# Kernel tuning notes

Measured on AMD Instinct MI355X. Metric: run time of the kernel, lower is better.

## Reference

```python
import jax, jax.numpy as jnp
import numpy as np


def setup_inputs() -> dict:
    key = jax.random.key(0)
    ks = jax.random.split(key, 5)
    t, b, s, d = 4, 4, 1024, 512
    x = jax.random.normal(ks[0], (t, b, s, d), dtype=jnp.float32)
    wq = jax.random.normal(ks[1], (d, d), dtype=jnp.float32) * 0.02
    wk = jax.random.normal(ks[2], (d, d), dtype=jnp.float32) * 0.02
    wv = jax.random.normal(ks[3], (d, d), dtype=jnp.float32) * 0.02
    wo = jax.random.normal(ks[4], (d, d), dtype=jnp.float32) * 0.02
    z = jnp.zeros((d,), dtype=jnp.float32)
    return {"x": x, "wq": wq, "bq": z, "wk": wk, "bk": z, "wv": wv,
            "bv": z, "wo": wo, "bo": z, "num_heads": 8}


def reference(x, wq, bq, wk, bk, wv, bv, wo, bo, num_heads):
    t, b, s, d = x.shape
    dh = d // num_heads
    # QKV projections (torch Linear stores weight as [out,in]; here weights are
    # random square matrices so x @ w + b is the same math)
    q = x @ wq + bq
    k = x @ wk + bk
    v = x @ wv + bv
    # Faithful to source: plain row-major view to (t*b*h, s, dh) WITHOUT
    # transposing a head axis (this mixes seq blocks into the batch-of-heads dim)
    q = q.reshape(t * b * num_heads, s, dh)
    k = k.reshape(t * b * num_heads, s, dh)
    v = v.reshape(t * b * num_heads, s, dh)
    scale = 1.0 / jnp.sqrt(jnp.float32(dh))
    scores = jnp.einsum('bqd,bkd->bqk', q, k) * scale  # [t*b*h, s, s]
    attn = jax.nn.softmax(scores, axis=-1)
    out = jnp.einsum('bqk,bkd->bqd', attn, v)  # [t*b*h, s, dh]
    out = out.reshape(t, b, s, d)
    return out @ wo + bo
```

## Files before the change

kernel.cpp:

```cpp
#include <hip/hip_runtime.h>

typedef __bf16 bf16;
typedef __bf16 bf16x4 __attribute__((ext_vector_type(4)));
typedef __bf16 bf16x8 __attribute__((ext_vector_type(8)));
typedef float  f32x4  __attribute__((ext_vector_type(4)));

#define MFMA16(a, b, c) __builtin_amdgcn_mfma_f32_16x16x32_bf16((a), (b), (c), 0, 0, 0)
#define SW(row, g) (((row) << 6) + ((((g) ^ ((row) & 7))) << 3))

#define QSCALE 0.1803368801111137f

typedef __attribute__((address_space(3))) uint32_t       lds_u32_t;
typedef const __attribute__((address_space(1))) uint32_t glob_u32_t;

__device__ __forceinline__ void ld_lds16(const bf16* g, bf16* l) {
    __builtin_amdgcn_global_load_lds((glob_u32_t*)g, (lds_u32_t*)l, 16, 0, 0);
}

__global__ __launch_bounds__(256) void prep(
    const float* __restrict__ X,
    const float* __restrict__ wq, const float* __restrict__ wk,
    const float* __restrict__ wv, const float* __restrict__ wo,
    bf16* __restrict__ Xb, bf16* __restrict__ wqkvT, bf16* __restrict__ woT)
{
    int bid = blockIdx.x;
    if (bid < 4096) {
        size_t i = ((size_t)bid * 256 + threadIdx.x) * 8;
        const f32x4* s = (const f32x4*)(X + i);
        f32x4 a = s[0], b = s[1];
        bf16x8 o;
        for (int e = 0; e < 4; e++) { o[e] = (bf16)a[e]; o[e + 4] = (bf16)b[e]; }
        *(bf16x8*)(Xb + i) = o;
    } else {
        int idx = (bid - 4096) * 256 + threadIdx.x;
        int which = idx >> 15;
        int r = idx & 32767;
        int kg = r >> 9, n = r & 511;
        const float* w = (which == 0) ? wq : (which == 1) ? wk : (which == 2) ? wv : wo;
        bf16x8 o;
        for (int e = 0; e < 8; e++) o[e] = (bf16)w[(size_t)(kg * 8 + e) * 512 + n];
        bf16* dst = ((which < 3) ? (wqkvT + (size_t)which * 262144) : woT) + (size_t)n * 512 + kg * 8;
        *(bf16x8*)dst = o;
    }
}

__global__ __launch_bounds__(256, 4) void gemm_qkv(
    const bf16* __restrict__ Xb, const bf16* __restrict__ WT,
    const float* __restrict__ bq, const float* __restrict__ bk,
    const float* __restrict__ bv,
    bf16* __restrict__ Q, bf16* __restrict__ K, bf16* __restrict__ V)
{
    __shared__ char smem[34816];
    bf16* As = (bf16*)smem;
    bf16* Bs = (bf16*)(smem + 16384);

    const int t = threadIdx.x;
    const int lane = t & 63, wid = t >> 6;
    const int wr = wid >> 1, wc = wid & 1;
    const int lr = lane & 15, quad = lane >> 4;
    const int bid = blockIdx.x;
    const int xcd = bid & 7, j0 = bid >> 3;
    const int m0 = (xcd * 16 + (j0 & 15)) * 128;
    const int x = j0 >> 4;
    const int which = x >> 2;
    const int n0 = (x & 3) * 128;
    const bf16* Wt = WT + (size_t)which * 262144;

    f32x4 zf = {0.f, 0.f, 0.f, 0.f};
    f32x4 acc[4][4];
    for (int i = 0; i < 4; i++)
        for (int jj = 0; jj < 4; jj++) acc[i][jj] = zf;

    const int srow = t >> 3;
    const int sg = (t & 7) ^ (srow & 7);
    const bf16* gA = Xb + (size_t)(m0 + srow) * 512 + sg * 8;
    const bf16* gB = Wt + (size_t)(n0 + srow) * 512 + sg * 8;
    bf16* lA = As + t * 8;
    bf16* lB = Bs + t * 8;

    for (int k0 = 0; k0 < 512; k0 += 64) {
        for (int p = 0; p < 4; p++) {
            ld_lds16(gA + k0 + p * 32 * 512, lA + p * 2048);
            ld_lds16(gB + k0 + p * 32 * 512, lB + p * 2048);
        }
        __syncthreads();
        for (int kk = 0; kk < 2; ++kk) {
            bf16x8 af[4], bf_[4];
            for (int i = 0; i < 4; i++)
                af[i] = *(const bf16x8*)&As[SW(wr * 64 + i * 16 + lr, kk * 4 + quad)];
            for (int jj = 0; jj < 4; jj++)
                bf_[jj] = *(const bf16x8*)&Bs[SW(wc * 64 + jj * 16 + lr, kk * 4 + quad)];
            for (int i = 0; i < 4; i++)
                for (int jj = 0; jj < 4; jj++)
                    acc[i][jj] = MFMA16(af[i], bf_[jj], acc[i][jj]);
        }
        __syncthreads();
    }

    bf16* OUT = (which == 0) ? Q : (which == 1) ? K : V;
    const float* bias = (which == 0) ? bq : (which == 1) ? bk : bv;
    const float qs = (which == 0) ? QSCALE : 1.0f;

    bf16* Ep = (bf16*)smem + wid * 4352;
    for (int jj = 0; jj < 4; jj++) {
        int n = n0 + wc * 64 + jj * 16 + lr;
        float bb = bias[n];
        for (int i = 0; i < 4; i++) {
            int row = i * 16 + quad * 4;
            for (int r = 0; r < 4; r++)
                Ep[(row + r) * 68 + jj * 16 + lr] = (bf16)((acc[i][jj][r] + bb) * qs);
        }
    }
    bf16* wO = OUT + (size_t)(m0 + wr * 64) * 512 + n0 + wc * 64;
    for (int s = 0; s < 8; s++) {
        int row = s * 8 + (lane >> 3), g = lane & 7;
        *(bf16x8*)(wO + (size_t)row * 512 + g * 8) = *(const bf16x8*)&Ep[row * 68 + g * 8];
    }
}

__global__ __launch_bounds__(256, 4) void gemm_out(
    const bf16* __restrict__ A, const bf16* __restrict__ WoT,
    const float* __restrict__ bo, float* __restrict__ OUT)
{
    __shared__ char smem[34816];
    bf16* As = (bf16*)smem;
    bf16* Bs = (bf16*)(smem + 16384);

    const int t = threadIdx.x;
    const int lane = t & 63, wid = t >> 6;
    const int wr = wid >> 1, wc = wid & 1;
    const int lr = lane & 15, quad = lane >> 4;
    const int bid = blockIdx.x;
    const int xcd = bid & 7, j0 = bid >> 3;
    const int m0 = (xcd * 16 + (j0 & 15)) * 128;
    const int n0 = (j0 >> 4) * 128;

    f32x4 zf = {0.f, 0.f, 0.f, 0.f};
    f32x4 acc[4][4];
    for (int i = 0; i < 4; i++)
        for (int jj = 0; jj < 4; jj++) acc[i][jj] = zf;

    const int srow = t >> 3;
    const int sg = (t & 7) ^ (srow & 7);
    const bf16* gA = A + (size_t)(m0 + srow) * 512 + sg * 8;
    const bf16* gB = WoT + (size_t)(n0 + srow) * 512 + sg * 8;
    bf16* lA = As + t * 8;
    bf16* lB = Bs + t * 8;

    for (int k0 = 0; k0 < 512; k0 += 64) {
        for (int p = 0; p < 4; p++) {
            ld_lds16(gA + k0 + p * 32 * 512, lA + p * 2048);
            ld_lds16(gB + k0 + p * 32 * 512, lB + p * 2048);
        }
        __syncthreads();
        for (int kk = 0; kk < 2; ++kk) {
            bf16x8 af[4], bf_[4];
            for (int i = 0; i < 4; i++)
                af[i] = *(const bf16x8*)&As[SW(wr * 64 + i * 16 + lr, kk * 4 + quad)];
            for (int jj = 0; jj < 4; jj++)
                bf_[jj] = *(const bf16x8*)&Bs[SW(wc * 64 + jj * 16 + lr, kk * 4 + quad)];
            for (int i = 0; i < 4; i++)
                for (int jj = 0; jj < 4; jj++)
                    acc[i][jj] = MFMA16(af[i], bf_[jj], acc[i][jj]);
        }
        __syncthreads();
    }

    float bb[4];
    for (int jj = 0; jj < 4; jj++) bb[jj] = bo[n0 + wc * 64 + jj * 16 + lr];

    float* Ef = (float*)smem + wid * 2112;
    for (int h = 0; h < 2; h++) {
        for (int jj = 0; jj < 4; jj++)
            for (int ii = 0; ii < 2; ii++) {
                int i = h * 2 + ii;
                int row = ii * 16 + quad * 4;
                for (int r = 0; r < 4; r++)
                    Ef[(row + r) * 66 + jj * 16 + lr] = acc[i][jj][r] + bb[jj];
            }
        float* wO = OUT + (size_t)(m0 + wr * 64 + h * 32) * 512 + n0 + wc * 64;
        for (int s = 0; s < 8; s++) {
            int row = s * 4 + (lane >> 4), c = (lane & 15) * 4;
            *(f32x4*)(wO + (size_t)row * 512 + c) = *(const f32x4*)&Ef[row * 66 + c];
        }
        __syncthreads();
    }
}

__global__ __launch_bounds__(256) void transpose_v(
    const bf16* __restrict__ V, bf16* __restrict__ VT)
{
    __shared__ bf16 L[64 * 72];
    const int t = threadIdx.x;
    const int b = blockIdx.y, kb = blockIdx.x;
    const bf16* src = V + ((size_t)b * 1024 + (size_t)kb * 64) * 64;
    const int row = t >> 2, c0 = (t & 3) * 16;
    *(bf16x8*)&L[row * 72 + c0]     = *(const bf16x8*)(src + row * 64 + c0);
    *(bf16x8*)&L[row * 72 + c0 + 8] = *(const bf16x8*)(src + row * 64 + c0 + 8);
    __syncthreads();
    bf16x8 o0, o1;
    for (int e = 0; e < 8; e++) {
        o0[e] = L[(c0 + e) * 72 + row];
        o1[e] = L[(c0 + 8 + e) * 72 + row];
    }
    bf16* dst = VT + ((size_t)b * 64 + row) * 1024 + (size_t)kb * 64 + c0;
    *(bf16x8*)dst       = o0;
    *(bf16x8*)(dst + 8) = o1;
}

__global__ __launch_bounds__(256, 4) void attn(
    const bf16* __restrict__ Q, const bf16* __restrict__ K,
    const bf16* __restrict__ VT, bf16* __restrict__ O)
{
    __shared__ char smem[32768];
    bf16* Kt = (bf16*)smem;
    bf16* Vt = (bf16*)(smem + 8192);
    bf16* Pt = (bf16*)(smem + 16384);

    const int t = threadIdx.x, lane = t & 63, wid = t >> 6;
    const int lr = lane & 15, quad = lane >> 4;
    const int bid = blockIdx.x;
    const int batch = (bid & 7) * 16 + ((bid >> 3) & 15);
    const int q0 = (bid >> 7) * 128;
    const bf16* Qb = Q + (size_t)batch * 65536;
    const bf16* Kb = K + (size_t)batch * 65536;
    const bf16* Vb = VT + (size_t)batch * 65536;

    bf16x8 qf[2][2];
    for (int jt = 0; jt < 2; jt++)
        for (int kk = 0; kk < 2; kk++)
            qf[jt][kk] = *(const bf16x8*)(Qb + (size_t)(q0 + wid * 32 + jt * 16 + lr) * 64 + kk * 32 + quad * 8);

    float lsum[2] = {0.f, 0.f};
    f32x4 zf = {0.f, 0.f, 0.f, 0.f};
    f32x4 oacc[2][4];
    for (int a = 0; a < 2; a++)
        for (int b = 0; b < 4; b++) oacc[a][b] = zf;

    const int vrow = t >> 2, vg = (t & 3) * 2;
    const bf16* gK = Kb + (size_t)vrow * 64 + (t & 3) * 16;
    const bf16* gV = Vb + (size_t)vrow * 1024 + (t & 3) * 16;

    bf16x8 kr0 = ((const bf16x8*)gK)[0], kr1 = ((const bf16x8*)gK)[1];
    bf16x8 vr0 = ((const bf16x8*)gV)[0], vr1 = ((const bf16x8*)gV)[1];

    for (int kt = 0; kt < 16; ++kt) {
        __syncthreads();
        *(bf16x8*)&Kt[SW(vrow, vg)]     = kr0;
        *(bf16x8*)&Kt[SW(vrow, vg + 1)] = kr1;
        *(bf16x8*)&Vt[SW(vrow, vg)]     = vr0;
        *(bf16x8*)&Vt[SW(vrow, vg + 1)] = vr1;
        __syncthreads();

        if (kt < 15) {
            const bf16x8* nK = (const bf16x8*)(gK + (kt + 1) * 4096);
            const bf16x8* nV = (const bf16x8*)(gV + (kt + 1) * 64);
            kr0 = nK[0]; kr1 = nK[1];
            vr0 = nV[0]; vr1 = nV[1];
        }

        f32x4 sacc[4][2];
        for (int i = 0; i < 4; i++)
            for (int jt = 0; jt < 2; jt++) sacc[i][jt] = zf;
        for (int kk = 0; kk < 2; ++kk) {
            bf16x8 af[4];
            for (int i = 0; i < 4; i++)
                af[i] = *(const bf16x8*)&Kt[SW(i * 16 + lr, kk * 4 + quad)];
            for (int i = 0; i < 4; i++)
                for (int jt = 0; jt < 2; jt++)
                    sacc[i][jt] = MFMA16(af[i], qf[jt][kk], sacc[i][jt]);
        }

        for (int jt = 0; jt < 2; jt++) {
            const int qrow = wid * 32 + jt * 16 + lr;
            const int pbase = (qrow << 6) + (quad & 1) * 4;
            float ss = 0.f;
            for (int i = 0; i < 4; i++) {
                bf16x4 pb;
                for (int r = 0; r < 4; r++) {
                    float p = __builtin_amdgcn_exp2f(sacc[i][jt][r]);
                    ss += p;
                    pb[r] = (bf16)p;
                }
                *(bf16x4*)&Pt[pbase + ((((i * 2 + (quad >> 1)) ^ (qrow & 7))) << 3)] = pb;
            }
            lsum[jt] += ss;
        }

        for (int kk = 0; kk < 2; ++kk) {
            bf16x8 ap[2], bv_[4];
            for (int mt = 0; mt < 2; mt++)
                ap[mt] = *(const bf16x8*)&Pt[SW(wid * 32 + mt * 16 + lr, kk * 4 + quad)];
            for (int nt = 0; nt < 4; nt++)
                bv_[nt] = *(const bf16x8*)&Vt[SW(nt * 16 + lr, kk * 4 + quad)];
            for (int mt = 0; mt < 2; mt++)
                for (int nt = 0; nt < 4; nt++)
                    oacc[mt][nt] = MFMA16(ap[mt], bv_[nt], oacc[mt][nt]);
        }
    }

    for (int jt = 0; jt < 2; jt++) {
        lsum[jt] += __shfl_xor(lsum[jt], 16, 64);
        lsum[jt] += __shfl_xor(lsum[jt], 32, 64);
    }
    float invl[2] = {1.f / lsum[0], 1.f / lsum[1]};

    __syncthreads();
    bf16* Ep = (bf16*)smem + wid * 2176;
    for (int mt = 0; mt < 2; mt++)
        for (int r = 0; r < 4; r++) {
            float im = __shfl(invl[mt], quad * 4 + r, 64);
            int row = mt * 16 + quad * 4 + r;
            for (int nt = 0; nt < 4; nt++)
                Ep[row * 68 + nt * 16 + lr] = (bf16)(oacc[mt][nt][r] * im);
        }
    bf16* Ob = O + (size_t)batch * 65536 + (size_t)(q0 + wid * 32) * 64;
    for (int s = 0; s < 4; s++) {
        int row = s * 8 + (lane >> 3), g = lane & 7;
        *(bf16x8*)(Ob + (size_t)row * 64 + g * 8) = *(const bf16x8*)&Ep[row * 68 + g * 8];
    }
}

extern "C" void kernel_launch(void* const* d_in, const int* in_sizes, int n_in,
                              void* d_out, int out_size, void* d_ws, size_t ws_size,
                              hipStream_t stream)
{
    const float* x  = (const float*)d_in[0];
    const float* wq = (const float*)d_in[1];
    const float* bq = (const float*)d_in[2];
    const float* wk = (const float*)d_in[3];
    const float* bk = (const float*)d_in[4];
    const float* wv = (const float*)d_in[5];
    const float* bv = (const float*)d_in[6];
    const float* wo = (const float*)d_in[7];
    const float* bo = (const float*)d_in[8];

    char* ws = (char*)d_ws;
    bf16* wqkvT = (bf16*)ws;
    bf16* woT   = (bf16*)(ws + 1572864);
    bf16* Xb    = (bf16*)(ws + 2097152);
    bf16* VTb   = Xb;
    bf16* Qb    = (bf16*)(ws + 2097152 + 16777216ull);
    bf16* Kb    = (bf16*)(ws + 2097152 + 2 * 16777216ull);
    bf16* Vb    = (bf16*)(ws + 2097152 + 3 * 16777216ull);
    bf16* Ab    = Vb;

    prep<<<4608, 256, 0, stream>>>(x, wq, wk, wv, wo, Xb, wqkvT, woT);
    gemm_qkv<<<1536, 256, 0, stream>>>(Xb, wqkvT, bq, bk, bv, Qb, Kb, Vb);
    transpose_v<<<dim3(16, 128), 256, 0, stream>>>(Vb, VTb);
    attn<<<1024, 256, 0, stream>>>(Qb, Kb, VTb, Ab);
    gemm_out<<<512, 256, 0, stream>>>(Ab, woT, bo, (float*)d_out);
}
```

Baseline: 198.4 us.

## Fuse V transpose and output projection into attention kernel

Removes the separate transpose_v and gemm_out kernels. V is now transposed while being stored to LDS inside the attention loop, and each attention block applies the Wo projection to its 128x64 output tile, which maps to 16 full tokens by 512 features. This cuts two launches and the global round trips for VT and the attention output. In exchange, each block streams all of WoT directly from global memory without LDS staging, adds scalar LDS stores for the V transpose, and keeps 16 A-fragments in registers, which may hurt occupancy.

```diff
diff --git a/kernel.cpp b/kernel.cpp
--- a/kernel.cpp
+++ b/kernel.cpp
@@ -118,99 +118,10 @@
     }
 }
 
-__global__ __launch_bounds__(256, 4) void gemm_out(
-    const bf16* __restrict__ A, const bf16* __restrict__ WoT,
+__global__ __launch_bounds__(256, 4) void attn_fused(
+    const bf16* __restrict__ Q, const bf16* __restrict__ K,
+    const bf16* __restrict__ V, const bf16* __restrict__ WoT,
     const float* __restrict__ bo, float* __restrict__ OUT)
-{
-    __shared__ char smem[34816];
-    bf16* As = (bf16*)smem;
-    bf16* Bs = (bf16*)(smem + 16384);
-
-    const int t = threadIdx.x;
-    const int lane = t & 63, wid = t >> 6;
-    const int wr = wid >> 1, wc = wid & 1;
-    const int lr = lane & 15, quad = lane >> 4;
-    const int bid = blockIdx.x;
-    const int xcd = bid & 7, j0 = bid >> 3;
-    const int m0 = (xcd * 16 + (j0 & 15)) * 128;
-    const int n0 = (j0 >> 4) * 128;
-
-    f32x4 zf = {0.f, 0.f, 0.f, 0.f};
-    f32x4 acc[4][4];
-    for (int i = 0; i < 4; i++)
-        for (int jj = 0; jj < 4; jj++) acc[i][jj] = zf;
-
-    const int srow = t >> 3;
-    const int sg = (t & 7) ^ (srow & 7);
-    const bf16* gA = A + (size_t)(m0 + srow) * 512 + sg * 8;
-    const bf16* gB = WoT + (size_t)(n0 + srow) * 512 + sg * 8;
-    bf16* lA = As + t * 8;
-    bf16* lB = Bs + t * 8;
-
-    for (int k0 = 0; k0 < 512; k0 += 64) {
-        for (int p = 0; p < 4; p++) {
-            ld_lds16(gA + k0 + p * 32 * 512, lA + p * 2048);
-            ld_lds16(gB + k0 + p * 32 * 512, lB + p * 2048);
-        }
-        __syncthreads();
-        for (int kk = 0; kk < 2; ++kk) {
-            bf16x8 af[4], bf_[4];
-            for (int i = 0; i < 4; i++)
-                af[i] = *(const bf16x8*)&As[SW(wr * 64 + i * 16 + lr, kk * 4 + quad)];
-            for (int jj = 0; jj < 4; jj++)
-                bf_[jj] = *(const bf16x8*)&Bs[SW(wc * 64 + jj * 16 + lr, kk * 4 + quad)];
-            for (int i = 0; i < 4; i++)
-                for (int jj = 0; jj < 4; jj++)
-                    acc[i][jj] = MFMA16(af[i], bf_[jj], acc[i][jj]);
-        }
-        __syncthreads();
-    }
-
-    float bb[4];
-    for (int jj = 0; jj < 4; jj++) bb[jj] = bo[n0 + wc * 64 + jj * 16 + lr];
-
-    float* Ef = (float*)smem + wid * 2112;
-    for (int h = 0; h < 2; h++) {
-        for (int jj = 0; jj < 4; jj++)
-            for (int ii = 0; ii < 2; ii++) {
-                int i = h * 2 + ii;
-                int row = ii * 16 + quad * 4;
-                for (int r = 0; r < 4; r++)
-                    Ef[(row + r) * 66 + jj * 16 + lr] = acc[i][jj][r] + bb[jj];
-            }
-        float* wO = OUT + (size_t)(m0 + wr * 64 + h * 32) * 512 + n0 + wc * 64;
-        for (int s = 0; s < 8; s++) {
-            int row = s * 4 + (lane >> 4), c = (lane & 15) * 4;
-            *(f32x4*)(wO + (size_t)row * 512 + c) = *(const f32x4*)&Ef[row * 66 + c];
-        }
-        __syncthreads();
-    }
-}
-
-__global__ __launch_bounds__(256) void transpose_v(
-    const bf16* __restrict__ V, bf16* __restrict__ VT)
-{
-    __shared__ bf16 L[64 * 72];
-    const int t = threadIdx.x;
-    const int b = blockIdx.y, kb = blockIdx.x;
-    const bf16* src = V + ((size_t)b * 1024 + (size_t)kb * 64) * 64;
-    const int row = t >> 2, c0 = (t & 3) * 16;
-    *(bf16x8*)&L[row * 72 + c0]     = *(const bf16x8*)(src + row * 64 + c0);
-    *(bf16x8*)&L[row * 72 + c0 + 8] = *(const bf16x8*)(src + row * 64 + c0 + 8);
-    __syncthreads();
-    bf16x8 o0, o1;
-    for (int e = 0; e < 8; e++) {
-        o0[e] = L[(c0 + e) * 72 + row];
-        o1[e] = L[(c0 + 8 + e) * 72 + row];
-    }
-    bf16* dst = VT + ((size_t)b * 64 + row) * 1024 + (size_t)kb * 64 + c0;
-    *(bf16x8*)dst       = o0;
-    *(bf16x8*)(dst + 8) = o1;
-}
-
-__global__ __launch_bounds__(256, 4) void attn(
-    const bf16* __restrict__ Q, const bf16* __restrict__ K,
-    const bf16* __restrict__ VT, bf16* __restrict__ O)
 {
     __shared__ char smem[32768];
     bf16* Kt = (bf16*)smem;
@@ -224,7 +135,7 @@
     const int q0 = (bid >> 7) * 128;
     const bf16* Qb = Q + (size_t)batch * 65536;
     const bf16* Kb = K + (size_t)batch * 65536;
-    const bf16* Vb = VT + (size_t)batch * 65536;
+    const bf16* Vb = V + (size_t)batch * 65536;
 
     bf16x8 qf[2][2];
     for (int jt = 0; jt < 2; jt++)
@@ -237,9 +148,11 @@
     for (int a = 0; a < 2; a++)
         for (int b = 0; b < 4; b++) oacc[a][b] = zf;
 
-    const int vrow = t >> 2, vg = (t & 3) * 2;
-    const bf16* gK = Kb + (size_t)vrow * 64 + (t & 3) * 16;
-    const bf16* gV = Vb + (size_t)vrow * 1024 + (t & 3) * 16;
+    const int vrow = t >> 2;
+    const int d0 = (t & 3) * 16;
+    const int vg = (t & 3) * 2;
+    const bf16* gK = Kb + (size_t)vrow * 64 + d0;
+    const bf16* gV = Vb + (size_t)vrow * 64 + d0;
 
     bf16x8 kr0 = ((const bf16x8*)gK)[0], kr1 = ((const bf16x8*)gK)[1];
     bf16x8 vr0 = ((const bf16x8*)gV)[0], vr1 = ((const bf16x8*)gV)[1];
@@ -248,13 +161,17 @@
         __syncthreads();
         *(bf16x8*)&Kt[SW(vrow, vg)]     = kr0;
         *(bf16x8*)&Kt[SW(vrow, vg + 1)] = kr1;
-        *(bf16x8*)&Vt[SW(vrow, vg)]     = vr0;
-        *(bf16x8*)&Vt[SW(vrow, vg + 1)] = vr1;
+        #pragma unroll
+        for (int e = 0; e < 8; e++) {
+            int d1 = d0 + e, d2 = d0 + 8 + e;
+            Vt[(d1 << 6) + (((vrow >> 3) ^ (d1 & 7)) << 3) + (vrow & 7)] = vr0[e];
+            Vt[(d2 << 6) + (((vrow >> 3) ^ (d2 & 7)) << 3) + (vrow & 7)] = vr1[e];
+        }
         __syncthreads();
 
         if (kt < 15) {
             const bf16x8* nK = (const bf16x8*)(gK + (kt + 1) * 4096);
-            const bf16x8* nV = (const bf16x8*)(gV + (kt + 1) * 64);
+            const bf16x8* nV = (const bf16x8*)(gV + (kt + 1) * 4096);
             kr0 = nK[0]; kr1 = nK[1];
             vr0 = nV[0]; vr1 = nV[1];
         }
@@ -305,19 +222,52 @@
     }
     float invl[2] = {1.f / lsum[0], 1.f / lsum[1]};
 
-    __syncthreads();
-    bf16* Ep = (bf16*)smem + wid * 2176;
+    bf16* Ot = Pt;
     for (int mt = 0; mt < 2; mt++)
         for (int r = 0; r < 4; r++) {
             float im = __shfl(invl[mt], quad * 4 + r, 64);
-            int row = mt * 16 + quad * 4 + r;
-            for (int nt = 0; nt < 4; nt++)
-                Ep[row * 68 + nt * 16 + lr] = (bf16)(oacc[mt][nt][r] * im);
-        }
-    bf16* Ob = O + (size_t)batch * 65536 + (size_t)(q0 + wid * 32) * 64;
-    for (int s = 0; s < 4; s++) {
-        int row = s * 8 + (lane >> 3), g = lane & 7;
-        *(bf16x8*)(Ob + (size_t)row * 64 + g * 8) = *(const bf16x8*)&Ep[row * 68 + g * 8];
+            int q = wid * 32 + mt * 16 + quad * 4 + r;
+            int tl = q >> 3, ql = (q & 7) * 8;
+            for (int nt = 0; nt < 4; nt++) {
+                int d = nt * 16 + lr;
+                int g = ql + (d >> 3);
+                Ot[tl * 512 + ((g ^ (tl & 7)) << 3) + (d & 7)] = (bf16)(oacc[mt][nt][r] * im);
+            }
+        }
+    __syncthreads();
+
+    bf16x8 afr[16];
+    #pragma unroll
+    for (int kc = 0; kc < 16; kc++) {
+        int g = kc * 4 + quad;
+        afr[kc] = *(const bf16x8*)&Ot[lr * 512 + ((g ^ (lr & 7)) << 3)];
+    }
+    __syncthreads();
+
+    f32x4 cacc[8];
+    for (int nt = 0; nt < 8; nt++) cacc[nt] = zf;
+    const bf16* wrow = WoT + (size_t)(wid * 128 + lr) * 512 + quad * 8;
+    for (int kc = 0; kc < 16; kc++) {
+        #pragma unroll
+        for (int nt = 0; nt < 8; nt++) {
+            bf16x8 bfr = *(const bf16x8*)(wrow + (size_t)nt * 16 * 512 + kc * 32);
+            cacc[nt] = MFMA16(afr[kc], bfr, cacc[nt]);
+        }
+    }
+
+    float* Ew = (float*)(smem + wid * 8192);
+    for (int nt = 0; nt < 8; nt++) {
+        float bb = bo[wid * 128 + nt * 16 + lr];
+        for (int r = 0; r < 4; r++) {
+            int tok = quad * 4 + r;
+            Ew[tok * 128 + nt * 16 + lr] = cacc[nt][r] + bb;
+        }
+    }
+    const int base = batch * 128 + (bid >> 7) * 16;
+    float* wOut = OUT + (size_t)base * 512 + wid * 128;
+    for (int s = 0; s < 8; s++) {
+        int tok = s * 2 + (lane >> 5), cg = lane & 31;
+        *(f32x4*)(wOut + (size_t)tok * 512 + cg * 4) = *(const f32x4*)&Ew[tok * 128 + cg * 4];
     }
 }
 
@@ -339,15 +289,11 @@
     bf16* wqkvT = (bf16*)ws;
     bf16* woT   = (bf16*)(ws + 1572864);
     bf16* Xb    = (bf16*)(ws + 2097152);
-    bf16* VTb   = Xb;
     bf16* Qb    = (bf16*)(ws + 2097152 + 16777216ull);
     bf16* Kb    = (bf16*)(ws + 2097152 + 2 * 16777216ull);
     bf16* Vb    = (bf16*)(ws + 2097152 + 3 * 16777216ull);
-    bf16* Ab    = Vb;
 
     prep<<<4608, 256, 0, stream>>>(x, wq, wk, wv, wo, Xb, wqkvT, woT);
     gemm_qkv<<<1536, 256, 0, stream>>>(Xb, wqkvT, bq, bk, bv, Qb, Kb, Vb);
-    transpose_v<<<dim3(16, 128), 256, 0, stream>>>(Vb, VTb);
-    attn<<<1024, 256, 0, stream>>>(Qb, Kb, VTb, Ab);
-    gemm_out<<<512, 256, 0, stream>>>(Ab, woT, bo, (float*)d_out);
-}
+    attn_fused<<<1024, 256, 0, stream>>>(Qb, Kb, Vb, woT, bo, (float*)d_out);
+}
```

Result: slower. 223.3 us (+12.5%).

## Load K and V fragments directly from global memory, dropping LDS staging

Applied to the files above, without the earlier changes.

The attention kernel no longer stages K and V tiles through shared memory with block-wide barriers. Each wave now loads its MFMA operand fragments for K and transposed V straight from global memory into registers. LDS shrinks to the per-wave P buffer, and the epilogue reuses that buffer with an XOR swizzle instead of padding. This removes two __syncthreads per key tile and the LDS round trip, and lowers LDS use, which may allow more resident blocks. The cost is that each of the four waves fetches the same K/V data separately, relying on cache, and the next tile is no longer prefetched into registers, so global load latency is exposed.

```diff
diff --git a/kernel.cpp b/kernel.cpp
--- a/kernel.cpp
+++ b/kernel.cpp
@@ -212,10 +212,8 @@
     const bf16* __restrict__ Q, const bf16* __restrict__ K,
     const bf16* __restrict__ VT, bf16* __restrict__ O)
 {
-    __shared__ char smem[32768];
-    bf16* Kt = (bf16*)smem;
-    bf16* Vt = (bf16*)(smem + 8192);
-    bf16* Pt = (bf16*)(smem + 16384);
+    __shared__ char smem[16384];
+    bf16* Pt = (bf16*)smem;
 
     const int t = threadIdx.x, lane = t & 63, wid = t >> 6;
     const int lr = lane & 15, quad = lane >> 4;
@@ -237,39 +235,34 @@
     for (int a = 0; a < 2; a++)
         for (int b = 0; b < 4; b++) oacc[a][b] = zf;
 
-    const int vrow = t >> 2, vg = (t & 3) * 2;
-    const bf16* gK = Kb + (size_t)vrow * 64 + (t & 3) * 16;
-    const bf16* gV = Vb + (size_t)vrow * 1024 + (t & 3) * 16;
-
-    bf16x8 kr0 = ((const bf16x8*)gK)[0], kr1 = ((const bf16x8*)gK)[1];
-    bf16x8 vr0 = ((const bf16x8*)gV)[0], vr1 = ((const bf16x8*)gV)[1];
+    const bf16* kbase = Kb + (size_t)lr * 64 + quad * 8;
+    const bf16* vbase = Vb + (size_t)lr * 1024 + quad * 8;
 
     for (int kt = 0; kt < 16; ++kt) {
-        __syncthreads();
-        *(bf16x8*)&Kt[SW(vrow, vg)]     = kr0;
-        *(bf16x8*)&Kt[SW(vrow, vg + 1)] = kr1;
-        *(bf16x8*)&Vt[SW(vrow, vg)]     = vr0;
-        *(bf16x8*)&Vt[SW(vrow, vg + 1)] = vr1;
-        __syncthreads();
-
-        if (kt < 15) {
-            const bf16x8* nK = (const bf16x8*)(gK + (kt + 1) * 4096);
-            const bf16x8* nV = (const bf16x8*)(gV + (kt + 1) * 64);
-            kr0 = nK[0]; kr1 = nK[1];
-            vr0 = nV[0]; vr1 = nV[1];
-        }
+        const int key0 = kt * 64;
+
+        bf16x8 af[2][4];
+        #pragma unroll
+        for (int kk = 0; kk < 2; ++kk)
+            #pragma unroll
+            for (int i = 0; i < 4; i++)
+                af[kk][i] = *(const bf16x8*)(kbase + (size_t)(key0 + i * 16) * 64 + kk * 32);
 
         f32x4 sacc[4][2];
         for (int i = 0; i < 4; i++)
             for (int jt = 0; jt < 2; jt++) sacc[i][jt] = zf;
-        for (int kk = 0; kk < 2; ++kk) {
-            bf16x8 af[4];
-            for (int i = 0; i < 4; i++)
-                af[i] = *(const bf16x8*)&Kt[SW(i * 16 + lr, kk * 4 + quad)];
+        #pragma unroll
+        for (int kk = 0; kk < 2; ++kk)
             for (int i = 0; i < 4; i++)
                 for (int jt = 0; jt < 2; jt++)
-                    sacc[i][jt] = MFMA16(af[i], qf[jt][kk], sacc[i][jt]);
-        }
+                    sacc[i][jt] = MFMA16(af[kk][i], qf[jt][kk], sacc[i][jt]);
+
+        bf16x8 bv_[2][4];
+        #pragma unroll
+        for (int kk = 0; kk < 2; ++kk)
+            #pragma unroll
+            for (int nt = 0; nt < 4; nt++)
+                bv_[kk][nt] = *(const bf16x8*)(vbase + (size_t)nt * 16384 + key0 + kk * 32);
 
         for (int jt = 0; jt < 2; jt++) {
             const int qrow = wid * 32 + jt * 16 + lr;
@@ -287,15 +280,14 @@
             lsum[jt] += ss;
         }
 
+        #pragma unroll
         for (int kk = 0; kk < 2; ++kk) {
-            bf16x8 ap[2], bv_[4];
+            bf16x8 ap[2];
             for (int mt = 0; mt < 2; mt++)
                 ap[mt] = *(const bf16x8*)&Pt[SW(wid * 32 + mt * 16 + lr, kk * 4 + quad)];
-            for (int nt = 0; nt < 4; nt++)
-                bv_[nt] = *(const bf16x8*)&Vt[SW(nt * 16 + lr, kk * 4 + quad)];
             for (int mt = 0; mt < 2; mt++)
                 for (int nt = 0; nt < 4; nt++)
-                    oacc[mt][nt] = MFMA16(ap[mt], bv_[nt], oacc[mt][nt]);
+                    oacc[mt][nt] = MFMA16(ap[mt], bv_[kk][nt], oacc[mt][nt]);
         }
     }
 
@@ -305,19 +297,21 @@
     }
     float invl[2] = {1.f / lsum[0], 1.f / lsum[1]};
 
-    __syncthreads();
-    bf16* Ep = (bf16*)smem + wid * 2176;
+    bf16* Ep = Pt + wid * 2048;
     for (int mt = 0; mt < 2; mt++)
         for (int r = 0; r < 4; r++) {
             float im = __shfl(invl[mt], quad * 4 + r, 64);
             int row = mt * 16 + quad * 4 + r;
-            for (int nt = 0; nt < 4; nt++)
-                Ep[row * 68 + nt * 16 + lr] = (bf16)(oacc[mt][nt][r] * im);
+            for (int nt = 0; nt < 4; nt++) {
+                int g = nt * 2 + (lr >> 3);
+                Ep[(row << 6) + ((g ^ (row & 7)) << 3) + (lr & 7)] = (bf16)(oacc[mt][nt][r] * im);
+            }
         }
     bf16* Ob = O + (size_t)batch * 65536 + (size_t)(q0 + wid * 32) * 64;
     for (int s = 0; s < 4; s++) {
         int row = s * 8 + (lane >> 3), g = lane & 7;
-        *(bf16x8*)(Ob + (size_t)row * 64 + g * 8) = *(const bf16x8*)&Ep[row * 68 + g * 8];
+        *(bf16x8*)(Ob + (size_t)row * 64 + g * 8) =
+            *(const bf16x8*)&Ep[(row << 6) + ((g ^ (row & 7)) << 3)];
     }
 }
 
```

New measurement: 274.7 us. +38.4%, slower.

## Fuse X fp32-to-bf16 conversion into QKV GEMM and reorder block mapping

Applied to the files above, without the earlier changes.

Removes the separate pass that converted X to bf16 in the prep kernel. The QKV GEMM now loads fp32 X directly, converts it in registers and writes swizzled bf16 into LDS, while the weight tiles still use async global-to-LDS loads. The block index mapping changes so the 12 N-tiles of one M-tile run consecutively, which improves reuse of the same X rows in cache. The trade-off is that each X tile is read as fp32 twelve times, doubling those bytes, and the A loads now go through registers instead of direct-to-LDS.

```diff
diff --git a/kernel.cpp b/kernel.cpp
--- a/kernel.cpp
+++ b/kernel.cpp
@@ -17,35 +17,24 @@
     __builtin_amdgcn_global_load_lds((glob_u32_t*)g, (lds_u32_t*)l, 16, 0, 0);
 }
 
-__global__ __launch_bounds__(256) void prep(
-    const float* __restrict__ X,
+__global__ __launch_bounds__(256) void prep_w(
     const float* __restrict__ wq, const float* __restrict__ wk,
     const float* __restrict__ wv, const float* __restrict__ wo,
-    bf16* __restrict__ Xb, bf16* __restrict__ wqkvT, bf16* __restrict__ woT)
-{
-    int bid = blockIdx.x;
-    if (bid < 4096) {
-        size_t i = ((size_t)bid * 256 + threadIdx.x) * 8;
-        const f32x4* s = (const f32x4*)(X + i);
-        f32x4 a = s[0], b = s[1];
-        bf16x8 o;
-        for (int e = 0; e < 4; e++) { o[e] = (bf16)a[e]; o[e + 4] = (bf16)b[e]; }
-        *(bf16x8*)(Xb + i) = o;
-    } else {
-        int idx = (bid - 4096) * 256 + threadIdx.x;
-        int which = idx >> 15;
-        int r = idx & 32767;
-        int kg = r >> 9, n = r & 511;
-        const float* w = (which == 0) ? wq : (which == 1) ? wk : (which == 2) ? wv : wo;
-        bf16x8 o;
-        for (int e = 0; e < 8; e++) o[e] = (bf16)w[(size_t)(kg * 8 + e) * 512 + n];
-        bf16* dst = ((which < 3) ? (wqkvT + (size_t)which * 262144) : woT) + (size_t)n * 512 + kg * 8;
-        *(bf16x8*)dst = o;
-    }
+    bf16* __restrict__ wqkvT, bf16* __restrict__ woT)
+{
+    int idx = blockIdx.x * 256 + threadIdx.x;
+    int which = idx >> 15;
+    int r = idx & 32767;
+    int kg = r >> 9, n = r & 511;
+    const float* w = (which == 0) ? wq : (which == 1) ? wk : (which == 2) ? wv : wo;
+    bf16x8 o;
+    for (int e = 0; e < 8; e++) o[e] = (bf16)w[(size_t)(kg * 8 + e) * 512 + n];
+    bf16* dst = ((which < 3) ? (wqkvT + (size_t)which * 262144) : woT) + (size_t)n * 512 + kg * 8;
+    *(bf16x8*)dst = o;
 }
 
 __global__ __launch_bounds__(256, 4) void gemm_qkv(
-    const bf16* __restrict__ Xb, const bf16* __restrict__ WT,
+    const float* __restrict__ X, const bf16* __restrict__ WT,
     const float* __restrict__ bq, const float* __restrict__ bk,
     const float* __restrict__ bv,
     bf16* __restrict__ Q, bf16* __restrict__ K, bf16* __restrict__ V)
@@ -60,8 +49,9 @@
     const int lr = lane & 15, quad = lane >> 4;
     const int bid = blockIdx.x;
     const int xcd = bid & 7, j0 = bid >> 3;
-    const int m0 = (xcd * 16 + (j0 & 15)) * 128;
-    const int x = j0 >> 4;
+    const int msub = j0 / 12;
+    const int x = j0 - msub * 12;
+    const int m0 = (xcd * 16 + msub) * 128;
     const int which = x >> 2;
     const int n0 = (x & 3) * 128;
     const bf16* Wt = WT + (size_t)which * 262144;
@@ -71,17 +61,22 @@
     for (int i = 0; i < 4; i++)
         for (int jj = 0; jj < 4; jj++) acc[i][jj] = zf;
 
-    const int srow = t >> 3;
-    const int sg = (t & 7) ^ (srow & 7);
-    const bf16* gA = Xb + (size_t)(m0 + srow) * 512 + sg * 8;
-    const bf16* gB = Wt + (size_t)(n0 + srow) * 512 + sg * 8;
-    bf16* lA = As + t * 8;
+    const int arow = t >> 3, ag = t & 7;
+    const float* gX = X + (size_t)(m0 + arow) * 512 + ag * 8;
+    const int sg = ag ^ (arow & 7);
+    const bf16* gB = Wt + (size_t)(n0 + arow) * 512 + sg * 8;
     bf16* lB = Bs + t * 8;
 
     for (int k0 = 0; k0 < 512; k0 += 64) {
+        for (int p = 0; p < 4; p++)
+            ld_lds16(gB + k0 + p * 32 * 512, lB + p * 2048);
+        #pragma unroll
         for (int p = 0; p < 4; p++) {
-            ld_lds16(gA + k0 + p * 32 * 512, lA + p * 2048);
-            ld_lds16(gB + k0 + p * 32 * 512, lB + p * 2048);
+            const f32x4* s = (const f32x4*)(gX + (size_t)(p * 32) * 512 + k0);
+            f32x4 a = s[0], b = s[1];
+            bf16x8 o;
+            for (int e = 0; e < 4; e++) { o[e] = (bf16)a[e]; o[e + 4] = (bf16)b[e]; }
+            *(bf16x8*)&As[SW(arow + p * 32, ag)] = o;
         }
         __syncthreads();
         for (int kk = 0; kk < 2; ++kk) {
@@ -338,15 +333,14 @@
     char* ws = (char*)d_ws;
     bf16* wqkvT = (bf16*)ws;
     bf16* woT   = (bf16*)(ws + 1572864);
-    bf16* Xb    = (bf16*)(ws + 2097152);
-    bf16* VTb   = Xb;
-    bf16* Qb    = (bf16*)(ws + 2097152 + 16777216ull);
-    bf16* Kb    = (bf16*)(ws + 2097152 + 2 * 16777216ull);
-    bf16* Vb    = (bf16*)(ws + 2097152 + 3 * 16777216ull);
+    bf16* Qb    = (bf16*)(ws + 2097152);
+    bf16* Kb    = (bf16*)(ws + 2097152 + 16777216ull);
+    bf16* Vb    = (bf16*)(ws + 2097152 + 2 * 16777216ull);
+    bf16* VTb   = (bf16*)(ws + 2097152 + 3 * 16777216ull);
     bf16* Ab    = Vb;
 
-    prep<<<4608, 256, 0, stream>>>(x, wq, wk, wv, wo, Xb, wqkvT, woT);
-    gemm_qkv<<<1536, 256, 0, stream>>>(Xb, wqkvT, bq, bk, bv, Qb, Kb, Vb);
+    prep_w<<<512, 256, 0, stream>>>(wq, wk, wv, wo, wqkvT, woT);
+    gemm_qkv<<<1536, 256, 0, stream>>>(x, wqkvT, bq, bk, bv, Qb, Kb, Vb);
     transpose_v<<<dim3(16, 128), 256, 0, stream>>>(Vb, VTb);
     attn<<<1024, 256, 0, stream>>>(Qb, Kb, VTb, Ab);
     gemm_out<<<512, 256, 0, stream>>>(Ab, woT, bo, (float*)d_out);
```

After: 210.2 us. +5.9%, slower.
